# Optimization experiments

Measured on AMD Instinct MI355X. Metric: run time of the kernel, lower is better.

## Reference

```python
import jax, jax.numpy as jnp
import numpy as np

B, T, D, U, C = 256, 512, 128, 128, 64


def setup_inputs() -> dict:
    key = jax.random.key(0)
    ks = jax.random.split(key, 4)
    s_in = 1.0 / np.sqrt(D)
    s_u = 1.0 / np.sqrt(U)
    return {
        "inputs": jax.random.normal(ks[0], (B, T, D), dtype=jnp.float32),
        "W1": jax.random.normal(ks[1], (D, U), dtype=jnp.float32) * s_in,
        "b1": jnp.zeros((U,), dtype=jnp.float32),
        "W2": jax.random.normal(ks[2], (U, U), dtype=jnp.float32) * s_u,
        "b2": jnp.zeros((U,), dtype=jnp.float32),
        "Wc": jax.random.normal(ks[3], (U, C), dtype=jnp.float32) * s_u,
        "bc": jnp.zeros((C,), dtype=jnp.float32),
    }


def reference(inputs, W1, b1, W2, b2, Wc, bc):
    # state_{t} = tanh(x_t @ W1 + b1) + tanh(state_{t-1} @ W2 + b2)
    # Input projection has no recurrent dependency -> precompute in one big GEMM.
    h = jnp.tanh(jnp.einsum("btd,du->btu", inputs, W1) + b1)  # (B, T, U)

    def step(state, h_t):
        y = h_t + jnp.tanh(state @ W2 + b2)  # (B, U)
        return y, y

    state0 = jnp.zeros((inputs.shape[0], W2.shape[0]), dtype=inputs.dtype)
    _, ys = jax.lax.scan(step, state0, jnp.swapaxes(h, 0, 1))  # ys: (T, B, U)
    features = jnp.swapaxes(ys, 0, 1)  # (B, T, U)
    # classifier: Dense head applied to stacked features
    return jnp.einsum("btu,uc->btc", features, Wc) + bc
```

## Files before the change

kernel.cpp:

```cpp
#include <hip/hip_runtime.h>

#define NB 256
#define NT 512
#define ND 128
#define NU 128
#define NC 64
#define NM (NB * NT)
#define YP 136

typedef _Float16 half2v __attribute__((ext_vector_type(2)));
typedef _Float16 half4v __attribute__((ext_vector_type(4)));
typedef _Float16 half8v __attribute__((ext_vector_type(8)));
typedef float f32x4 __attribute__((ext_vector_type(4)));
typedef float v2f __attribute__((ext_vector_type(2)));

#define MFMA(a, b, c) __builtin_amdgcn_mfma_f32_16x16x32_f16((a), (b), (c), 0, 0, 0)

__device__ __forceinline__ half2v pk2(float a, float b) {
  return __builtin_bit_cast(half2v, __builtin_amdgcn_cvt_pkrtz(a, b));
}

__device__ __forceinline__ float tanh_s(float s) {
  float e = __expf(s);
  return fmaf(-2.0f, __builtin_amdgcn_rcpf(e + 1.0f), 1.0f);
}

__device__ __forceinline__ void wg_barrier() {
  asm volatile("s_waitcnt lgkmcnt(0)\n\ts_barrier" ::: "memory");
}

__global__ __launch_bounds__(256, 1) void k1_inproj(
    const float* __restrict__ x, const float* __restrict__ W1,
    const float* __restrict__ b1v, _Float16* __restrict__ TH)
{
  __shared__ _Float16 W1T[ND * YP];
  const int tid = (int)threadIdx.x;
  for (int i = tid; i < ND * NU; i += 256) {
    int k = i >> 7, n = i & 127;
    W1T[n * YP + k] = (_Float16)(2.0f * W1[i]);
  }
  __syncthreads();

  const int L = tid & 63, wv = tid >> 6;
  const int v = L & 15, q = L >> 4;
  const int m0 = (int)blockIdx.x * 64 + wv * 16;

  const float* xr = x + (size_t)(m0 + v) * ND + 8 * q;
  half8v xf[4];
#pragma unroll
  for (int kk = 0; kk < 4; ++kk) {
    float4 a = *(const float4*)(xr + 32 * kk);
    float4 b = *(const float4*)(xr + 32 * kk + 4);
    half2v p0 = pk2(a.x, a.y), p1 = pk2(a.z, a.w);
    half2v p2 = pk2(b.x, b.y), p3 = pk2(b.z, b.w);
    xf[kk] = (half8v){p0[0], p0[1], p1[0], p1[1], p2[0], p2[1], p3[0], p3[1]};
  }

#pragma unroll
  for (int ht = 0; ht < 8; ++ht) {
    f32x4 acc;
    {
      float4 bb = *(const float4*)&b1v[16 * ht + 4 * q];
      acc = (f32x4){2.f * bb.x, 2.f * bb.y, 2.f * bb.z, 2.f * bb.w};
    }
#pragma unroll
    for (int kk = 0; kk < 4; ++kk) {
      half8v wa = *(const half8v*)&W1T[(16 * ht + v) * YP + 32 * kk + 8 * q];
      acc = MFMA(wa, xf[kk], acc);
    }
    half2v zlo = pk2(tanh_s(acc[0]), tanh_s(acc[1]));
    half2v zhi = pk2(tanh_s(acc[2]), tanh_s(acc[3]));
    half4v z = {zlo[0], zlo[1], zhi[0], zhi[1]};
    *(half4v*)&TH[(size_t)(m0 + v) * NU + 16 * ht + 4 * q] = z;
  }
}

__global__ __launch_bounds__(512, 1) void k2_recur(
    const _Float16* __restrict__ TH, const float* __restrict__ W2,
    const float* __restrict__ b2v, _Float16* __restrict__ Yws)
{
  __shared__ _Float16 Ybuf[2][16 * YP];

  const int tid = (int)threadIdx.x;
  const int w = tid >> 6;
  const int L = tid & 63;
  const int v = L & 15, q = L >> 4;
  const int b0 = (int)blockIdx.x * 16;

  half8v w2f[4];
#pragma unroll
  for (int kk = 0; kk < 4; ++kk) {
    half8v h;
#pragma unroll
    for (int j = 0; j < 8; ++j)
      h[j] = (_Float16)(2.0f * W2[(size_t)(32 * kk + 8 * q + j) * NU + 16 * w + v]);
    w2f[kk] = h;
  }
  f32x4 b2f;
  {
    float4 bb = *(const float4*)&b2v[16 * w + 4 * q];
    b2f = (f32x4){2.f * bb.x, 2.f * bb.y, 2.f * bb.z, 2.f * bb.w};
  }

  const _Float16* thp = TH + (size_t)(b0 + v) * NT * NU + 16 * w + 4 * q;
  _Float16* yp = Yws + (size_t)(b0 + v) * NT * NU + 16 * w + 4 * q;

  half4v thr0 = *(const half4v*)(thp + 0 * NU);
  half4v thr1 = *(const half4v*)(thp + 1 * NU);
  half4v thr2 = *(const half4v*)(thp + 2 * NU);
  half4v thr3 = *(const half4v*)(thp + 3 * NU);

  f32x4 racc = b2f;
  _Float16* wr = &Ybuf[0][0] + v * YP + 16 * w + 4 * q;
  const _Float16* rd = &Ybuf[0][0] + v * YP + 8 * q;

#define K2STEP(T_, THR_, BUF_)                                                \
  {                                                                           \
    const int t_ = (T_);                                                      \
    half2v zlo = pk2(tanh_s(racc[0]), tanh_s(racc[1]));                       \
    half2v zhi = pk2(tanh_s(racc[2]), tanh_s(racc[3]));                       \
    half2v tlo = __builtin_shufflevector(THR_, THR_, 0, 1);                   \
    half2v thi = __builtin_shufflevector(THR_, THR_, 2, 3);                   \
    half2v ylo = zlo + tlo;                                                   \
    half2v yhi = zhi + thi;                                                   \
    half4v y4 = {ylo[0], ylo[1], yhi[0], yhi[1]};                             \
    *(half4v*)(wr + (BUF_) * (16 * YP)) = y4;                                 \
    *(half4v*)(yp + (size_t)t_ * NU) = y4;         \
    {                                                                         \
      int tn = t_ + 4; tn = tn < NT ? tn : NT - 1;                            \
      THR_ = *(const half4v*)(thp + (size_t)tn * NU);                         \
    }                                                                         \
    wg_barrier();                                                             \
    half8v yf0 = *(const half8v*)(rd + (BUF_) * (16 * YP) + 0);               \
    half8v yf1 = *(const half8v*)(rd + (BUF_) * (16 * YP) + 32);              \
    half8v yf2 = *(const half8v*)(rd + (BUF_) * (16 * YP) + 64);              \
    half8v yf3 = *(const half8v*)(rd + (BUF_) * (16 * YP) + 96);              \
    racc = b2f;                                                               \
    racc = MFMA(w2f[0], yf0, racc);                                           \
    racc = MFMA(w2f[1], yf1, racc);                                           \
    racc = MFMA(w2f[2], yf2, racc);                                           \
    racc = MFMA(w2f[3], yf3, racc);                                           \
  }

#pragma unroll 1
  for (int t = 0; t < NT; t += 4) {
    K2STEP(t + 0, thr0, 0)
    K2STEP(t + 1, thr1, 1)
    K2STEP(t + 2, thr2, 0)
    K2STEP(t + 3, thr3, 1)
  }
}

__global__ __launch_bounds__(256, 1) void k3_head(
    const _Float16* __restrict__ Y, const float* __restrict__ Wc,
    const float* __restrict__ bcv, float* __restrict__ out)
{
  __shared__ _Float16 WcT[NC * YP];
  const int tid = (int)threadIdx.x;
  for (int i = tid; i < NU * NC; i += 256) {
    int k = i >> 6, c = i & 63;
    WcT[c * YP + k] = (_Float16)Wc[i];
  }
  __syncthreads();

  const int L = tid & 63, wv = tid >> 6;
  const int v = L & 15, q = L >> 4;
  const int m0 = (int)blockIdx.x * 64 + wv * 16;

  const _Float16* yr = Y + (size_t)(m0 + v) * NU + 8 * q;
  half8v yf[4];
#pragma unroll
  for (int kk = 0; kk < 4; ++kk) yf[kk] = *(const half8v*)(yr + 32 * kk);

  float* op = out + (size_t)(m0 + v) * NC + 4 * q;
#pragma unroll
  for (int ct = 0; ct < 4; ++ct) {
    f32x4 acc;
    {
      float4 bb = *(const float4*)&bcv[16 * ct + 4 * q];
      acc = (f32x4){bb.x, bb.y, bb.z, bb.w};
    }
#pragma unroll
    for (int kk = 0; kk < 4; ++kk) {
      half8v wa = *(const half8v*)&WcT[(16 * ct + v) * YP + 32 * kk + 8 * q];
      acc = MFMA(wa, yf[kk], acc);
    }
    *(float4*)(op + 16 * ct) = (float4){acc[0], acc[1], acc[2], acc[3]};
  }
}

__device__ __forceinline__ float fast_tanh(float x) {
  float e = __expf(2.0f * x);
  return 1.0f - 2.0f / (e + 1.0f);
}
__device__ __forceinline__ float bcast(float val, int i) {
  return __builtin_bit_cast(float, __builtin_amdgcn_readlane(__builtin_bit_cast(int, val), i));
}

__global__ __launch_bounds__(256, 1) void rnn_fallback(
    const float* __restrict__ x, const float* __restrict__ W1,
    const float* __restrict__ b1v, const float* __restrict__ W2,
    const float* __restrict__ b2v, const float* __restrict__ Wc,
    const float* __restrict__ bcv, float* __restrict__ out)
{
  __shared__ float xring[16][ND];
  __shared__ float pH[2][4][NU];
  __shared__ float pR[2][4][NU];
  __shared__ float pC[2][4][NC];

  const int tid  = (int)threadIdx.x;
  const int lane = tid & 63;
  const int kg   = tid >> 6;
  const int b    = (int)blockIdx.x;
  const float4* xr4 = (const float4*)(x + (size_t)b * NT * ND);

  v2f w1f[32], w2f[32];
  float wcf[32];
#pragma unroll
  for (int i = 0; i < 32; ++i) {
    int k = kg * 32 + i;
    w1f[i] = (v2f){W1[k * NU + lane], W1[k * NU + lane + 64]};
    w2f[i] = (v2f){W2[k * NU + lane], W2[k * NU + lane + 64]};
    wcf[i] = Wc[k * NC + lane];
  }
  const float biasc = bcv[lane];
  float bias1 = 0.f, bias2 = 0.f;
  if (lane < 32) { bias1 = b1v[kg * 32 + lane]; bias2 = b2v[kg * 32 + lane]; }

  float4 stg = make_float4(0.f, 0.f, 0.f, 0.f);
  if (lane < 32) {
    float4 a0 = xr4[(kg + 0) * 32 + lane];
    float4 a1 = xr4[(kg + 4) * 32 + lane];
    ((float4*)xring[kg + 0])[lane] = a0;
    ((float4*)xring[kg + 4])[lane] = a1;
    stg = xr4[(kg + 8) * 32 + lane];
  }
  float yseg = 0.f;
  wg_barrier();

  for (int t = 0; t < NT; ++t) {
    const int pb = t & 1;
    v2f accH0 = {0.f, 0.f}, accH1 = {0.f, 0.f};
    const float4* xb = (const float4*)&xring[t & 15][kg * 32];
#pragma unroll
    for (int i = 0; i < 4; ++i) {
      float4 xa = xb[2 * i];
      float4 xc = xb[2 * i + 1];
      accH0 = w1f[8*i+0] * (v2f){xa.x, xa.x} + accH0;
      accH1 = w1f[8*i+1] * (v2f){xa.y, xa.y} + accH1;
      accH0 = w1f[8*i+2] * (v2f){xa.z, xa.z} + accH0;
      accH1 = w1f[8*i+3] * (v2f){xa.w, xa.w} + accH1;
      accH0 = w1f[8*i+4] * (v2f){xc.x, xc.x} + accH0;
      accH1 = w1f[8*i+5] * (v2f){xc.y, xc.y} + accH1;
      accH0 = w1f[8*i+6] * (v2f){xc.z, xc.z} + accH0;
      accH1 = w1f[8*i+7] * (v2f){xc.w, xc.w} + accH1;
    }
    v2f accH = accH0 + accH1;
    v2f accR0 = {0.f, 0.f}, accR1 = {0.f, 0.f};
    float accC0 = 0.f, accC1 = 0.f;
#pragma unroll
    for (int i = 0; i < 16; ++i) {
      float s0 = bcast(yseg, 2 * i);
      float s1 = bcast(yseg, 2 * i + 1);
      accR0 = w2f[2*i+0] * (v2f){s0, s0} + accR0;
      accR1 = w2f[2*i+1] * (v2f){s1, s1} + accR1;
      accC0 = fmaf(s0, wcf[2*i+0], accC0);
      accC1 = fmaf(s1, wcf[2*i+1], accC1);
    }
    v2f accR = accR0 + accR1;
    float accC = accC0 + accC1;

    pH[pb][kg][lane]      = accH.x;
    pH[pb][kg][lane + 64] = accH.y;
    pR[pb][kg][lane]      = accR.x;
    pR[pb][kg][lane + 64] = accR.y;
    pC[pb][kg][lane]      = accC;

    if (kg == (t & 3)) {
      if (lane < 32) {
        ((float4*)xring[(t + 8) & 15])[lane] = stg;
        int r = t + 12; r = (r < NT) ? r : (NT - 1);
        stg = xr4[r * 32 + lane];
      }
    }
    wg_barrier();
    if (lane < 32) {
      const int j = kg * 32 + lane;
      float hs = bias1, rs = bias2;
#pragma unroll
      for (int g = 0; g < 4; ++g) { hs += pH[pb][g][j]; rs += pR[pb][g][j]; }
      yseg = fast_tanh(hs) + fast_tanh(rs);
    }
    if (kg == ((t + 2) & 3) && t >= 1) {
      float cs = biasc;
#pragma unroll
      for (int g = 0; g < 4; ++g) cs += pC[pb][g][lane];
      out[((size_t)b * NT + (t - 1)) * NC + lane] = cs;
    }
  }
  float accC0 = 0.f, accC1 = 0.f;
#pragma unroll
  for (int i = 0; i < 16; ++i) {
    float s0 = bcast(yseg, 2 * i);
    float s1 = bcast(yseg, 2 * i + 1);
    accC0 = fmaf(s0, wcf[2*i+0], accC0);
    accC1 = fmaf(s1, wcf[2*i+1], accC1);
  }
  pC[0][kg][lane] = accC0 + accC1;
  wg_barrier();
  if (kg == 0) {
    float cs = biasc;
#pragma unroll
    for (int g = 0; g < 4; ++g) cs += pC[0][g][lane];
    out[((size_t)b * NT + (NT - 1)) * NC + lane] = cs;
  }
}

extern "C" void kernel_launch(void* const* d_in, const int* in_sizes, int n_in,
                              void* d_out, int out_size, void* d_ws, size_t ws_size,
                              hipStream_t stream) {
  (void)in_sizes; (void)n_in; (void)out_size;
  const float* x   = (const float*)d_in[0];
  const float* W1  = (const float*)d_in[1];
  const float* b1v = (const float*)d_in[2];
  const float* W2  = (const float*)d_in[3];
  const float* b2v = (const float*)d_in[4];
  const float* Wc  = (const float*)d_in[5];
  const float* bcv = (const float*)d_in[6];
  float* out = (float*)d_out;

  const size_t need = (size_t)NM * NU * 2 * 2;
  if (ws_size >= need) {
    _Float16* TH = (_Float16*)d_ws;
    _Float16* Yw = TH + (size_t)NM * NU;
    hipLaunchKernelGGL(k1_inproj, dim3(NM / 64), dim3(256), 0, stream, x, W1, b1v, TH);
    hipLaunchKernelGGL(k2_recur, dim3(NB / 16), dim3(512), 0, stream, TH, W2, b2v, Yw);
    hipLaunchKernelGGL(k3_head, dim3(NM / 64), dim3(256), 0, stream, Yw, Wc, bcv, out);
  } else {
    hipLaunchKernelGGL(rnn_fallback, dim3(NB), dim3(256), 0, stream,
                       x, W1, b1v, W2, b2v, Wc, bcv, out);
  }
}
```

Measured before the change: 315.6 us.

## Halve recurrence waves with two column tiles each and chunk-major workspace layout

The recurrent kernel now uses 4 waves, each computing two 16-column output tiles with interleaved MFMA chains. This cuts barrier participants but doubles per-wave tanh and MFMA work on the serial path. The TH and Y workspaces are stored column-chunk-major so each wave's per-step loads and stores are contiguous. The input-projection and head kernels keep their weights in registers and loop over 4 row passes per block with fewer blocks.

```diff
diff --git a/kernel.cpp b/kernel.cpp
--- a/kernel.cpp
+++ b/kernel.cpp
@@ -29,7 +29,14 @@
   asm volatile("s_waitcnt lgkmcnt(0)\n\ts_barrier" ::: "memory");
 }
 
-__global__ __launch_bounds__(256, 1) void k1_inproj(
+__device__ __forceinline__ half8v cvt8(const float4& a, const float4& b) {
+  half2v p0 = pk2(a.x, a.y), p1 = pk2(a.z, a.w);
+  half2v p2 = pk2(b.x, b.y), p3 = pk2(b.z, b.w);
+  return (half8v){p0[0], p0[1], p1[0], p1[1], p2[0], p2[1], p3[0], p3[1]};
+}
+
+
+__global__ __launch_bounds__(256, 2) void k1_inproj(
     const float* __restrict__ x, const float* __restrict__ W1,
     const float* __restrict__ b1v, _Float16* __restrict__ TH)
 {
@@ -43,39 +50,45 @@
 
   const int L = tid & 63, wv = tid >> 6;
   const int v = L & 15, q = L >> 4;
-  const int m0 = (int)blockIdx.x * 64 + wv * 16;
-
-  const float* xr = x + (size_t)(m0 + v) * ND + 8 * q;
-  half8v xf[4];
-#pragma unroll
-  for (int kk = 0; kk < 4; ++kk) {
-    float4 a = *(const float4*)(xr + 32 * kk);
-    float4 b = *(const float4*)(xr + 32 * kk + 4);
-    half2v p0 = pk2(a.x, a.y), p1 = pk2(a.z, a.w);
-    half2v p2 = pk2(b.x, b.y), p3 = pk2(b.z, b.w);
-    xf[kk] = (half8v){p0[0], p0[1], p1[0], p1[1], p2[0], p2[1], p3[0], p3[1]};
-  }
-
+
+  half8v w1f[8][4];
+#pragma unroll
+  for (int ht = 0; ht < 8; ++ht)
+#pragma unroll
+    for (int kk = 0; kk < 4; ++kk)
+      w1f[ht][kk] = *(const half8v*)&W1T[(16 * ht + v) * YP + 32 * kk + 8 * q];
+  f32x4 b1f[8];
 #pragma unroll
   for (int ht = 0; ht < 8; ++ht) {
-    f32x4 acc;
-    {
-      float4 bb = *(const float4*)&b1v[16 * ht + 4 * q];
-      acc = (f32x4){2.f * bb.x, 2.f * bb.y, 2.f * bb.z, 2.f * bb.w};
-    }
+    float4 bb = *(const float4*)&b1v[16 * ht + 4 * q];
+    b1f[ht] = (f32x4){2.f * bb.x, 2.f * bb.y, 2.f * bb.z, 2.f * bb.w};
+  }
+
+#pragma unroll 1
+  for (int pass = 0; pass < 4; ++pass) {
+    const int m0 = (int)blockIdx.x * 256 + pass * 64 + wv * 16;
+    const float* xr = x + (size_t)(m0 + v) * ND + 8 * q;
+    half8v xf[4];
 #pragma unroll
     for (int kk = 0; kk < 4; ++kk) {
-      half8v wa = *(const half8v*)&W1T[(16 * ht + v) * YP + 32 * kk + 8 * q];
-      acc = MFMA(wa, xf[kk], acc);
-    }
-    half2v zlo = pk2(tanh_s(acc[0]), tanh_s(acc[1]));
-    half2v zhi = pk2(tanh_s(acc[2]), tanh_s(acc[3]));
-    half4v z = {zlo[0], zlo[1], zhi[0], zhi[1]};
-    *(half4v*)&TH[(size_t)(m0 + v) * NU + 16 * ht + 4 * q] = z;
-  }
-}
-
-__global__ __launch_bounds__(512, 1) void k2_recur(
+      float4 a = *(const float4*)(xr + 32 * kk);
+      float4 b = *(const float4*)(xr + 32 * kk + 4);
+      xf[kk] = cvt8(a, b);
+    }
+#pragma unroll
+    for (int ht = 0; ht < 8; ++ht) {
+      f32x4 acc = b1f[ht];
+#pragma unroll
+      for (int kk = 0; kk < 4; ++kk) acc = MFMA(w1f[ht][kk], xf[kk], acc);
+      half2v zlo = pk2(tanh_s(acc[0]), tanh_s(acc[1]));
+      half2v zhi = pk2(tanh_s(acc[2]), tanh_s(acc[3]));
+      half4v z = {zlo[0], zlo[1], zhi[0], zhi[1]};
+      *(half4v*)&TH[(size_t)ht * NM * 16 + (size_t)(m0 + v) * 16 + 4 * q] = z;
+    }
+  }
+}
+
+__global__ __launch_bounds__(256, 1) void k2_recur(
     const _Float16* __restrict__ TH, const float* __restrict__ W2,
     const float* __restrict__ b2v, _Float16* __restrict__ Yws)
 {
@@ -87,71 +100,86 @@
   const int v = L & 15, q = L >> 4;
   const int b0 = (int)blockIdx.x * 16;
 
-  half8v w2f[4];
-#pragma unroll
-  for (int kk = 0; kk < 4; ++kk) {
-    half8v h;
-#pragma unroll
-    for (int j = 0; j < 8; ++j)
-      h[j] = (_Float16)(2.0f * W2[(size_t)(32 * kk + 8 * q + j) * NU + 16 * w + v]);
-    w2f[kk] = h;
-  }
-  f32x4 b2f;
+  half8v w2f[2][4];
+#pragma unroll
+  for (int c = 0; c < 2; ++c)
+#pragma unroll
+    for (int kk = 0; kk < 4; ++kk) {
+      half8v h;
+#pragma unroll
+      for (int j = 0; j < 8; ++j)
+        h[j] = (_Float16)(2.0f * W2[(size_t)(32 * kk + 8 * q + j) * NU + 16 * (2 * w + c) + v]);
+      w2f[c][kk] = h;
+    }
+  f32x4 b2f0, b2f1;
   {
-    float4 bb = *(const float4*)&b2v[16 * w + 4 * q];
-    b2f = (f32x4){2.f * bb.x, 2.f * bb.y, 2.f * bb.z, 2.f * bb.w};
-  }
-
-  const _Float16* thp = TH + (size_t)(b0 + v) * NT * NU + 16 * w + 4 * q;
-  _Float16* yp = Yws + (size_t)(b0 + v) * NT * NU + 16 * w + 4 * q;
-
-  half4v thr0 = *(const half4v*)(thp + 0 * NU);
-  half4v thr1 = *(const half4v*)(thp + 1 * NU);
-  half4v thr2 = *(const half4v*)(thp + 2 * NU);
-  half4v thr3 = *(const half4v*)(thp + 3 * NU);
-
-  f32x4 racc = b2f;
-  _Float16* wr = &Ybuf[0][0] + v * YP + 16 * w + 4 * q;
+    float4 a = *(const float4*)&b2v[16 * (2 * w) + 4 * q];
+    float4 b = *(const float4*)&b2v[16 * (2 * w + 1) + 4 * q];
+    b2f0 = (f32x4){2.f * a.x, 2.f * a.y, 2.f * a.z, 2.f * a.w};
+    b2f1 = (f32x4){2.f * b.x, 2.f * b.y, 2.f * b.z, 2.f * b.w};
+  }
+
+  const _Float16* thp0 = TH + (size_t)(2 * w) * NM * 16 + (size_t)(b0 + v) * NT * 16 + 4 * q;
+  const _Float16* thp1 = thp0 + (size_t)NM * 16;
+  _Float16* ypw = Yws + (size_t)w * NM * 32 + (size_t)(b0 + v) * NT * 32 + 4 * q;
+
+  half4v th0[4], th1[4];
+#pragma unroll
+  for (int i = 0; i < 4; ++i) {
+    th0[i] = *(const half4v*)(thp0 + (size_t)i * 16);
+    th1[i] = *(const half4v*)(thp1 + (size_t)i * 16);
+  }
+
+  f32x4 racc0 = b2f0, racc1 = b2f1;
+  _Float16* wr = &Ybuf[0][0] + v * YP + 32 * w + 4 * q;
   const _Float16* rd = &Ybuf[0][0] + v * YP + 8 * q;
 
-#define K2STEP(T_, THR_, BUF_)                                                \
+#define K2STEP(T_, I_)                                                        \
   {                                                                           \
     const int t_ = (T_);                                                      \
-    half2v zlo = pk2(tanh_s(racc[0]), tanh_s(racc[1]));                       \
-    half2v zhi = pk2(tanh_s(racc[2]), tanh_s(racc[3]));                       \
-    half2v tlo = __builtin_shufflevector(THR_, THR_, 0, 1);                   \
-    half2v thi = __builtin_shufflevector(THR_, THR_, 2, 3);                   \
-    half2v ylo = zlo + tlo;                                                   \
-    half2v yhi = zhi + thi;                                                   \
-    half4v y4 = {ylo[0], ylo[1], yhi[0], yhi[1]};                             \
-    *(half4v*)(wr + (BUF_) * (16 * YP)) = y4;                                 \
-    *(half4v*)(yp + (size_t)t_ * NU) = y4;         \
+    const int bo_ = (t_ & 1) * (16 * YP);                                     \
+    half2v zlo0 = pk2(tanh_s(racc0[0]), tanh_s(racc0[1]));                    \
+    half2v zhi0 = pk2(tanh_s(racc0[2]), tanh_s(racc0[3]));                    \
+    half2v zlo1 = pk2(tanh_s(racc1[0]), tanh_s(racc1[1]));                    \
+    half2v zhi1 = pk2(tanh_s(racc1[2]), tanh_s(racc1[3]));                    \
+    half4v t40 = th0[I_], t41 = th1[I_];                                      \
+    half2v yl0 = zlo0 + (half2v){t40[0], t40[1]};                             \
+    half2v yh0 = zhi0 + (half2v){t40[2], t40[3]};                             \
+    half2v yl1 = zlo1 + (half2v){t41[0], t41[1]};                             \
+    half2v yh1 = zhi1 + (half2v){t41[2], t41[3]};                             \
+    half4v y0 = {yl0[0], yl0[1], yh0[0], yh0[1]};                             \
+    half4v y1 = {yl1[0], yl1[1], yh1[0], yh1[1]};                             \
+    *(half4v*)(wr + bo_) = y0;                                                \
+    *(half4v*)(wr + bo_ + 16) = y1;                                           \
+    *(half4v*)(ypw + (size_t)t_ * 32) = y0;              \
+    *(half4v*)(ypw + (size_t)t_ * 32 + 16) = y1;                              \
     {                                                                         \
       int tn = t_ + 4; tn = tn < NT ? tn : NT - 1;                            \
-      THR_ = *(const half4v*)(thp + (size_t)tn * NU);                         \
+      th0[I_] = *(const half4v*)(thp0 + (size_t)tn * 16);                     \
+      th1[I_] = *(const half4v*)(thp1 + (size_t)tn * 16);                     \
     }                                                                         \
     wg_barrier();                                                             \
-    half8v yf0 = *(const half8v*)(rd + (BUF_) * (16 * YP) + 0);               \
-    half8v yf1 = *(const half8v*)(rd + (BUF_) * (16 * YP) + 32);              \
-    half8v yf2 = *(const half8v*)(rd + (BUF_) * (16 * YP) + 64);              \
-    half8v yf3 = *(const half8v*)(rd + (BUF_) * (16 * YP) + 96);              \
-    racc = b2f;                                                               \
-    racc = MFMA(w2f[0], yf0, racc);                                           \
-    racc = MFMA(w2f[1], yf1, racc);                                           \
-    racc = MFMA(w2f[2], yf2, racc);                                           \
-    racc = MFMA(w2f[3], yf3, racc);                                           \
+    half8v yf0 = *(const half8v*)(rd + bo_ + 0);                              \
+    half8v yf1 = *(const half8v*)(rd + bo_ + 32);                             \
+    half8v yf2 = *(const half8v*)(rd + bo_ + 64);                             \
+    half8v yf3 = *(const half8v*)(rd + bo_ + 96);                             \
+    racc0 = b2f0;  racc1 = b2f1;                                              \
+    racc0 = MFMA(w2f[0][0], yf0, racc0);  racc1 = MFMA(w2f[1][0], yf0, racc1);\
+    racc0 = MFMA(w2f[0][1], yf1, racc0);  racc1 = MFMA(w2f[1][1], yf1, racc1);\
+    racc0 = MFMA(w2f[0][2], yf2, racc0);  racc1 = MFMA(w2f[1][2], yf2, racc1);\
+    racc0 = MFMA(w2f[0][3], yf3, racc0);  racc1 = MFMA(w2f[1][3], yf3, racc1);\
   }
 
 #pragma unroll 1
   for (int t = 0; t < NT; t += 4) {
-    K2STEP(t + 0, thr0, 0)
-    K2STEP(t + 1, thr1, 1)
-    K2STEP(t + 2, thr2, 0)
-    K2STEP(t + 3, thr3, 1)
-  }
-}
-
-__global__ __launch_bounds__(256, 1) void k3_head(
+    K2STEP(t + 0, 0)
+    K2STEP(t + 1, 1)
+    K2STEP(t + 2, 2)
+    K2STEP(t + 3, 3)
+  }
+}
+
+__global__ __launch_bounds__(256, 2) void k3_head(
     const _Float16* __restrict__ Y, const float* __restrict__ Wc,
     const float* __restrict__ bcv, float* __restrict__ out)
 {
@@ -165,27 +193,35 @@
 
   const int L = tid & 63, wv = tid >> 6;
   const int v = L & 15, q = L >> 4;
-  const int m0 = (int)blockIdx.x * 64 + wv * 16;
-
-  const _Float16* yr = Y + (size_t)(m0 + v) * NU + 8 * q;
-  half8v yf[4];
-#pragma unroll
-  for (int kk = 0; kk < 4; ++kk) yf[kk] = *(const half8v*)(yr + 32 * kk);
-
-  float* op = out + (size_t)(m0 + v) * NC + 4 * q;
+
+  half8v wcf[4][4];
+#pragma unroll
+  for (int ct = 0; ct < 4; ++ct)
+#pragma unroll
+    for (int kk = 0; kk < 4; ++kk)
+      wcf[ct][kk] = *(const half8v*)&WcT[(16 * ct + v) * YP + 32 * kk + 8 * q];
+  f32x4 bcf[4];
 #pragma unroll
   for (int ct = 0; ct < 4; ++ct) {
-    f32x4 acc;
-    {
-      float4 bb = *(const float4*)&bcv[16 * ct + 4 * q];
-      acc = (f32x4){bb.x, bb.y, bb.z, bb.w};
-    }
-#pragma unroll
-    for (int kk = 0; kk < 4; ++kk) {
-      half8v wa = *(const half8v*)&WcT[(16 * ct + v) * YP + 32 * kk + 8 * q];
-      acc = MFMA(wa, yf[kk], acc);
-    }
-    *(float4*)(op + 16 * ct) = (float4){acc[0], acc[1], acc[2], acc[3]};
+    float4 bb = *(const float4*)&bcv[16 * ct + 4 * q];
+    bcf[ct] = (f32x4){bb.x, bb.y, bb.z, bb.w};
+  }
+
+#pragma unroll 1
+  for (int pass = 0; pass < 4; ++pass) {
+    const int m0 = (int)blockIdx.x * 256 + pass * 64 + wv * 16;
+    half8v yf[4];
+#pragma unroll
+    for (int kk = 0; kk < 4; ++kk)
+      yf[kk] = *(const half8v*)(Y + (size_t)kk * NM * 32 + (size_t)(m0 + v) * 32 + 8 * q);
+    float* op = out + (size_t)(m0 + v) * NC + 4 * q;
+#pragma unroll
+    for (int ct = 0; ct < 4; ++ct) {
+      f32x4 acc = bcf[ct];
+#pragma unroll
+      for (int kk = 0; kk < 4; ++kk) acc = MFMA(wcf[ct][kk], yf[kk], acc);
+      *(float4*)(op + 16 * ct) = (float4){acc[0], acc[1], acc[2], acc[3]};
+    }
   }
 }
 
@@ -333,9 +369,9 @@
   if (ws_size >= need) {
     _Float16* TH = (_Float16*)d_ws;
     _Float16* Yw = TH + (size_t)NM * NU;
-    hipLaunchKernelGGL(k1_inproj, dim3(NM / 64), dim3(256), 0, stream, x, W1, b1v, TH);
-    hipLaunchKernelGGL(k2_recur, dim3(NB / 16), dim3(512), 0, stream, TH, W2, b2v, Yw);
-    hipLaunchKernelGGL(k3_head, dim3(NM / 64), dim3(256), 0, stream, Yw, Wc, bcv, out);
+    hipLaunchKernelGGL(k1_inproj, dim3(NM / 256), dim3(256), 0, stream, x, W1, b1v, TH);
+    hipLaunchKernelGGL(k2_recur, dim3(NB / 16), dim3(256), 0, stream, TH, W2, b2v, Yw);
+    hipLaunchKernelGGL(k3_head, dim3(NM / 256), dim3(256), 0, stream, Yw, Wc, bcv, out);
   } else {
     hipLaunchKernelGGL(rnn_fallback, dim3(NB), dim3(256), 0, stream,
                        x, W1, b1v, W2, b2v, Wc, bcv, out);
```

After: 315.9 us. About the same (+0.1%).
